# Kernel tuning notes

Hardware: AMD Instinct MI355X
Metric: run time of the kernel (lower is better)

## Reference

```python
import jax, jax.numpy as jnp
import numpy as np

N_NODES = 100000
N_EDGES = 1600000
IN_DIM, HID_DIM, OUT_DIM = 128, 128, 64


def setup_inputs() -> dict:
    key = jax.random.key(0)
    k1, k2, k3, k4 = jax.random.split(key, 4)
    x = jax.random.normal(k1, (N_NODES, IN_DIM), dtype=jnp.float32)
    edge_index = jax.random.randint(k2, (2, N_EDGES), 0, N_NODES, dtype=jnp.int32)
    # Glorot-ish init for weights
    W1 = jax.random.normal(k3, (IN_DIM, HID_DIM), dtype=jnp.float32) / np.sqrt(IN_DIM)
    W2 = jax.random.normal(k4, (HID_DIM, OUT_DIM), dtype=jnp.float32) / np.sqrt(HID_DIM)
    b1 = jnp.zeros((HID_DIM,), dtype=jnp.float32)
    b2 = jnp.zeros((OUT_DIM,), dtype=jnp.float32)
    return {"x": x, "edge_index": edge_index, "W1": W1, "b1": b1, "W2": W2, "b2": b2}


def _gcn_norm(edge_index, num_nodes):
    # PyG gcn_norm: add self-loops, symmetric normalization deg^-1/2 A deg^-1/2
    loops = jnp.arange(num_nodes, dtype=edge_index.dtype)
    src = jnp.concatenate([edge_index[0], loops])  # [E+N]
    tgt = jnp.concatenate([edge_index[1], loops])
    deg = jax.ops.segment_sum(jnp.ones_like(tgt, dtype=jnp.float32), tgt,
                              num_segments=num_nodes)
    dinv = jnp.where(deg > 0, jax.lax.rsqrt(deg), 0.0)
    norm = dinv[src] * dinv[tgt]  # [E+N]
    return src, tgt, norm


def _gcn_conv(x, W, b, src, tgt, norm, num_nodes):
    h = x @ W                              # [N, D_out] transform first (GCNConv order)
    msg = norm[:, None] * h[src]           # gather + scale per edge
    agg = jax.ops.segment_sum(msg, tgt, num_segments=num_nodes)  # scatter-add
    return agg + b


def reference(x, edge_index, W1, b1, W2, b2):
    n = x.shape[0]
    src, tgt, norm = _gcn_norm(edge_index, n)
    h = jax.nn.relu(_gcn_conv(x, W1, b1, src, tgt, norm, n))
    out = _gcn_conv(h, W2, b2, src, tgt, norm, n)
    return out
```

## Files before the change

### kernel.cpp

```cpp
#include <hip/hip_runtime.h>


typedef unsigned int uint;
typedef unsigned short ushort;
typedef __attribute__((ext_vector_type(8))) short bf16x8;
typedef __attribute__((ext_vector_type(4))) float f32x4;

#define BSHIFT 8
#define MAXBK  512
#define NB     256

__device__ inline ushort f2bf(float f) {
    uint u = __float_as_uint(f);
    return (ushort)((u + 0x7fffu + ((u >> 16) & 1u)) >> 16);
}
__device__ inline float bf_lo(uint u) { return __uint_as_float(u << 16); }
__device__ inline float bf_hi(uint u) { return __uint_as_float(u & 0xffff0000u); }

__global__ __launch_bounds__(256) void hist_kernel(const int* __restrict__ tgt,
                                                   int* __restrict__ counts,
                                                   int E, int chunk, int nbk) {
    __shared__ int hist[MAXBK];
    int t = threadIdx.x, b = blockIdx.x;
    for (int i = t; i < nbk; i += 256) hist[i] = 0;
    __syncthreads();
    int s = b * chunk, e = min(E, s + chunk);
    for (int i = s + t; i < e; i += 256) atomicAdd(&hist[tgt[i] >> BSHIFT], 1);
    __syncthreads();
    for (int i = t; i < nbk; i += 256) counts[i * NB + b] = hist[i];
}

__global__ __launch_bounds__(256) void scan_partial(const int* __restrict__ in,
                                                    int* __restrict__ bsum, int M) {
    int t = threadIdx.x, b = blockIdx.x;
    int base = b * 1024 + t * 4;
    int s = 0;
#pragma unroll
    for (int k = 0; k < 4; ++k) s += (base + k < M) ? in[base + k] : 0;
#pragma unroll
    for (int off = 32; off > 0; off >>= 1) s += __shfl_down(s, off, 64);
    __shared__ int ws[4];
    if ((t & 63) == 0) ws[t >> 6] = s;
    __syncthreads();
    if (t == 0) bsum[b] = ws[0] + ws[1] + ws[2] + ws[3];
}

__global__ __launch_bounds__(256) void scan_final_counts(int* __restrict__ counts,
                                                         const int* __restrict__ bsum,
                                                         int M) {
    int t = threadIdx.x, b = blockIdx.x;
    int lane = t & 63, wid = t >> 6;
    int p = 0;
    for (int i = t; i < b; i += 256) p += bsum[i];
#pragma unroll
    for (int off = 32; off > 0; off >>= 1) p += __shfl_down(p, off, 64);
    __shared__ int ps[4];
    if (lane == 0) ps[wid] = p;
    __syncthreads();
    int pre = ps[0] + ps[1] + ps[2] + ps[3];

    int base = b * 1024 + t * 4;
    int d[4];
#pragma unroll
    for (int k = 0; k < 4; ++k) d[k] = (base + k < M) ? counts[base + k] : 0;
    int tot = d[0] + d[1] + d[2] + d[3];
    int incl = tot;
#pragma unroll
    for (int off = 1; off < 64; off <<= 1) {
        int u = __shfl_up(incl, off, 64);
        if (lane >= off) incl += u;
    }
    __shared__ int wsum[4];
    if (lane == 63) wsum[wid] = incl;
    __syncthreads();
    int woff = 0;
    for (int w = 0; w < wid; ++w) woff += wsum[w];
    int run = incl - tot + woff + pre;
#pragma unroll
    for (int k = 0; k < 4; ++k) {
        if (base + k < M) counts[base + k] = run;
        run += d[k];
    }
}

__global__ __launch_bounds__(256) void bucket_scatter(const int* __restrict__ src,
                                                      const int* __restrict__ tgt,
                                                      const int* __restrict__ offsets,
                                                      int* __restrict__ tmpP,
                                                      int E, int chunk, int nbk) {
    __shared__ int cur[MAXBK];
    int t = threadIdx.x, b = blockIdx.x;
    for (int i = t; i < nbk; i += 256) cur[i] = offsets[i * NB + b];
    __syncthreads();
    int s = b * chunk, e = min(E, s + chunk);
    for (int i = s + t; i < e; i += 256) {
        int tg = tgt[i];
        int p = atomicAdd(&cur[tg >> BSHIFT], 1);
        tmpP[p] = (src[i] << BSHIFT) | (tg & 255);
    }
}

__global__ __launch_bounds__(256) void bucket_deg(const int* __restrict__ tmpP,
                                                  const int* __restrict__ offsets,
                                                  int* __restrict__ deg,
                                                  int N, int E, int nbk) {
    __shared__ int cnt[256];
    int t = threadIdx.x, b = blockIdx.x;
    cnt[t] = 0;
    __syncthreads();
    int s = offsets[b * NB];
    int e = (b + 1 < nbk) ? offsets[(b + 1) * NB] : E;
    for (int i = s + t; i < e; i += 256) atomicAdd(&cnt[tmpP[i] & 255], 1);
    __syncthreads();
    int node = b * 256 + t;
    if (node < N) deg[node] = cnt[t];
}

__global__ __launch_bounds__(256) void scan_final_deg(const int* __restrict__ deg,
                                                      const int* __restrict__ offsets,
                                                      int* __restrict__ rowptr,
                                                      float* __restrict__ dinv,
                                                      int N, int E) {
    int t = threadIdx.x, b = blockIdx.x;
    int lane = t & 63, wid = t >> 6;
    int pre = offsets[(4 * b) * NB];
    int base = b * 1024 + t * 4;
    int d[4];
#pragma unroll
    for (int k = 0; k < 4; ++k) d[k] = (base + k < N) ? deg[base + k] : 0;
    int tot = d[0] + d[1] + d[2] + d[3];
    int incl = tot;
#pragma unroll
    for (int off = 1; off < 64; off <<= 1) {
        int u = __shfl_up(incl, off, 64);
        if (lane >= off) incl += u;
    }
    __shared__ int wsum[4];
    if (lane == 63) wsum[wid] = incl;
    __syncthreads();
    int woff = 0;
    for (int w = 0; w < wid; ++w) woff += wsum[w];
    int run = incl - tot + woff + pre;
#pragma unroll
    for (int k = 0; k < 4; ++k) {
        if (base + k < N) {
            rowptr[base + k] = run;
            dinv[base + k] = rsqrtf((float)d[k] + 1.0f);
        }
        run += d[k];
    }
    if (b == gridDim.x - 1 && t == 255) rowptr[N] = E;
}

__global__ __launch_bounds__(256) void bucket_fill(const int* __restrict__ tmpP,
                                                   const int* __restrict__ rowptr,
                                                   int* __restrict__ csr_src, int N) {
    __shared__ int cur[256];
    int t = threadIdx.x, b = blockIdx.x;
    int base = b * 256;
    int node = base + t;
    if (node < N) cur[t] = rowptr[node];
    __syncthreads();
    int s = rowptr[base];
    int e = rowptr[min(base + 256, N)];
    for (int i = s + t; i < e; i += 256) {
        int ed = tmpP[i];
        int p = atomicAdd(&cur[ed & 255], 1);
        csr_src[p] = ed >> BSHIFT;
    }
}

template <int M>
__global__ __launch_bounds__(256) void gemm_mfma(const float* __restrict__ A,
                                                 const float* __restrict__ W,
                                                 ushort* __restrict__ C, int N) {
    constexpr int WTS = 136;
    __shared__ ushort WT[M * WTS];
    const int tid = threadIdx.x;
    for (int i = tid; i < 128 * (M / 4); i += 256) {
        int k = i / (M / 4);
        int n0 = (i % (M / 4)) * 4;
        float4 w = *(const float4*)&W[k * M + n0];
        WT[(n0 + 0) * WTS + k] = f2bf(w.x);
        WT[(n0 + 1) * WTS + k] = f2bf(w.y);
        WT[(n0 + 2) * WTS + k] = f2bf(w.z);
        WT[(n0 + 3) * WTS + k] = f2bf(w.w);
    }
    __syncthreads();

    const int wv = tid >> 6, lane = tid & 63;
    const int quad = lane >> 4, mrow = lane & 15;
    int arow_i = blockIdx.x * 64 + wv * 16 + mrow;
    if (arow_i >= N) arow_i = N - 1;
    const float* arow = &A[(size_t)arow_i * 128];

    f32x4 acc[M / 16];
#pragma unroll
    for (int t = 0; t < M / 16; ++t) acc[t] = (f32x4){0.f, 0.f, 0.f, 0.f};

#pragma unroll
    for (int ks = 0; ks < 4; ++ks) {
        const int k0 = ks * 32 + quad * 8;
        float4 a0 = *(const float4*)&arow[k0];
        float4 a1 = *(const float4*)&arow[k0 + 4];
        bf16x8 af;
        af[0] = (short)f2bf(a0.x); af[1] = (short)f2bf(a0.y);
        af[2] = (short)f2bf(a0.z); af[3] = (short)f2bf(a0.w);
        af[4] = (short)f2bf(a1.x); af[5] = (short)f2bf(a1.y);
        af[6] = (short)f2bf(a1.z); af[7] = (short)f2bf(a1.w);
#pragma unroll
        for (int t = 0; t < M / 16; ++t) {
            int n = t * 16 + mrow;
            bf16x8 bfr = *(const bf16x8*)&WT[n * WTS + k0];
            acc[t] = __builtin_amdgcn_mfma_f32_16x16x32_bf16(af, bfr, acc[t], 0, 0, 0);
        }
    }

    const int orow0 = blockIdx.x * 64 + wv * 16 + quad * 4;
#pragma unroll
    for (int r = 0; r < 4; ++r) {
        int orow = orow0 + r;
        if (orow < N) {
#pragma unroll
            for (int t = 0; t < M / 16; ++t)
                C[(size_t)orow * M + t * 16 + mrow] = f2bf(acc[t][r]);
        }
    }
}

template <int D, bool RELU>
__global__ __launch_bounds__(256) void gather_kernel(
    const ushort* __restrict__ h, const int* __restrict__ rowptr,
    const int* __restrict__ csr_src, const float* __restrict__ dinv,
    const float* __restrict__ bias, float* __restrict__ out, int N) {
    constexpr int Q = D / 8;
    constexpr int G = 64 / Q;
    const int wid = threadIdx.x >> 6, lane = threadIdx.x & 63;
    const int node = blockIdx.x * 4 + wid;
    if (node >= N) return;
    const int g = lane / Q, q = lane % Q;
    const int qoff = q * 8;
    const int beg = rowptr[node], end = rowptr[node + 1];
    float acc[8] = {};

    for (int j = beg; j < end; j += 2 * G) {
        int e0 = j + g, e1 = j + G + g;
        {
            bool v = e0 < end;
            int s = v ? csr_src[e0] : node;
            float w = v ? dinv[s] : 0.0f;
            uint4 hv = *(const uint4*)&h[(size_t)s * D + qoff];
            acc[0] += w * bf_lo(hv.x); acc[1] += w * bf_hi(hv.x);
            acc[2] += w * bf_lo(hv.y); acc[3] += w * bf_hi(hv.y);
            acc[4] += w * bf_lo(hv.z); acc[5] += w * bf_hi(hv.z);
            acc[6] += w * bf_lo(hv.w); acc[7] += w * bf_hi(hv.w);
        }
        {
            bool v = e1 < end;
            int s = v ? csr_src[e1] : node;
            float w = v ? dinv[s] : 0.0f;
            uint4 hv = *(const uint4*)&h[(size_t)s * D + qoff];
            acc[0] += w * bf_lo(hv.x); acc[1] += w * bf_hi(hv.x);
            acc[2] += w * bf_lo(hv.y); acc[3] += w * bf_hi(hv.y);
            acc[4] += w * bf_lo(hv.z); acc[5] += w * bf_hi(hv.z);
            acc[6] += w * bf_lo(hv.w); acc[7] += w * bf_hi(hv.w);
        }
    }
#pragma unroll
    for (int m = Q; m < 64; m <<= 1)
#pragma unroll
        for (int k = 0; k < 8; ++k) acc[k] += __shfl_xor(acc[k], m, 64);

    const float di = dinv[node];
    {
        uint4 hv = *(const uint4*)&h[(size_t)node * D + qoff];
        acc[0] += di * bf_lo(hv.x); acc[1] += di * bf_hi(hv.x);
        acc[2] += di * bf_lo(hv.y); acc[3] += di * bf_hi(hv.y);
        acc[4] += di * bf_lo(hv.z); acc[5] += di * bf_hi(hv.z);
        acc[6] += di * bf_lo(hv.w); acc[7] += di * bf_hi(hv.w);
    }
    if (g == 0) {
        float4 b0 = *(const float4*)&bias[qoff];
        float4 b1 = *(const float4*)&bias[qoff + 4];
        float r[8] = {di * acc[0] + b0.x, di * acc[1] + b0.y,
                      di * acc[2] + b0.z, di * acc[3] + b0.w,
                      di * acc[4] + b1.x, di * acc[5] + b1.y,
                      di * acc[6] + b1.z, di * acc[7] + b1.w};
        if (RELU) {
#pragma unroll
            for (int k = 0; k < 8; ++k) r[k] = fmaxf(r[k], 0.0f);
        }
        *(float4*)&out[(size_t)node * D + qoff]     = make_float4(r[0], r[1], r[2], r[3]);
        *(float4*)&out[(size_t)node * D + qoff + 4] = make_float4(r[4], r[5], r[6], r[7]);
    }
}

extern "C" void kernel_launch(void* const* d_in, const int* in_sizes, int n_in,
                              void* d_out, int out_size, void* d_ws, size_t ws_size,
                              hipStream_t stream) {
    const float* x  = (const float*)d_in[0];
    const int*   ei = (const int*)d_in[1];
    const float* W1 = (const float*)d_in[2];
    const float* b1 = (const float*)d_in[3];
    const float* W2 = (const float*)d_in[4];
    const float* b2 = (const float*)d_in[5];
    float* out = (float*)d_out;

    const int N = in_sizes[0] / 128;
    const int E = in_sizes[1] / 2;
    const int* src = ei;
    const int* tgt = ei + E;

    const int nbk   = (N + 255) >> BSHIFT;
    const int chunk = (E + NB - 1) / NB;
    const int Mc    = nbk * NB;

    float* ws = (float*)d_ws;
    const size_t Np = (size_t)((N + 3) & ~3);
    float*  dinv    = ws;
    int*    deg     = (int*)(ws + Np);
    int*    rowptr  = deg + Np;
    int*    counts  = rowptr + Np + 4;
    int*    bsum    = counts + MAXBK * NB;
    int*    csr_src = bsum + 128;
    int*    tmpP    = csr_src + E;
    ushort* h       = (ushort*)(tmpP + E);
    float*  h1      = (float*)(h + (size_t)N * 128);
    ushort* h2      = h;

    const int nbc = (Mc + 1023) / 1024;
    const int nbd = (N + 1023) / 1024;

    hist_kernel<<<NB, 256, 0, stream>>>(tgt, counts, E, chunk, nbk);
    scan_partial<<<nbc, 256, 0, stream>>>(counts, bsum, Mc);
    scan_final_counts<<<nbc, 256, 0, stream>>>(counts, bsum, Mc);
    bucket_scatter<<<NB, 256, 0, stream>>>(src, tgt, counts, tmpP, E, chunk, nbk);
    bucket_deg<<<nbk, 256, 0, stream>>>(tmpP, counts, deg, N, E, nbk);
    scan_final_deg<<<nbd, 256, 0, stream>>>(deg, counts, rowptr, dinv, N, E);
    bucket_fill<<<nbk, 256, 0, stream>>>(tmpP, rowptr, csr_src, N);

    gemm_mfma<128><<<(N + 63) / 64, 256, 0, stream>>>(x, W1, h, N);
    gather_kernel<128, true><<<(N + 3) / 4, 256, 0, stream>>>(
        h, rowptr, csr_src, dinv, b1, h1, N);

    gemm_mfma<64><<<(N + 63) / 64, 256, 0, stream>>>(h1, W2, h2, N);
    gather_kernel<64, false><<<(N + 3) / 4, 256, 0, stream>>>(
        h2, rowptr, csr_src, dinv, b2, out, N);
}
```

Measured before the change: 335.1 us.

## Fuse CSR build kernels and store hidden layer as bf16

Merges the per-bucket degree count, the degree scan and the CSR fill into one kernel that stages each bucket's packed edges in shared memory. This removes two launches and a second global read of the packed edges. The first-layer gather output is also written as bf16 instead of fp32 and read straight into the second GEMM, which roughly halves that intermediate's traffic and skips the conversion step. The large shared staging buffer lowers occupancy, and the extra bf16 rounding of the hidden activations adds some precision loss.

```diff
diff --git a/kernel.cpp b/kernel.cpp
--- a/kernel.cpp
+++ b/kernel.cpp
@@ -4,11 +4,13 @@
 typedef unsigned int uint;
 typedef unsigned short ushort;
 typedef __attribute__((ext_vector_type(8))) short bf16x8;
+typedef __attribute__((ext_vector_type(8))) ushort u16x8;
 typedef __attribute__((ext_vector_type(4))) float f32x4;
 
 #define BSHIFT 8
 #define MAXBK  512
 #define NB     256
+#define CAP    8192
 
 __device__ inline ushort f2bf(float f) {
     uint u = __float_as_uint(f);
@@ -100,78 +102,57 @@
     }
 }
 
-__global__ __launch_bounds__(256) void bucket_deg(const int* __restrict__ tmpP,
-                                                  const int* __restrict__ offsets,
-                                                  int* __restrict__ deg,
-                                                  int N, int E, int nbk) {
+__global__ __launch_bounds__(256) void bucket_finish(const int* __restrict__ tmpP,
+                                                     const int* __restrict__ offsets,
+                                                     int* __restrict__ rowptr,
+                                                     float* __restrict__ dinv,
+                                                     int* __restrict__ csr_src,
+                                                     int N, int E, int nbk) {
+    __shared__ int stage[CAP];
     __shared__ int cnt[256];
+    __shared__ int wsum[4];
     int t = threadIdx.x, b = blockIdx.x;
     cnt[t] = 0;
     __syncthreads();
     int s = offsets[b * NB];
     int e = (b + 1 < nbk) ? offsets[(b + 1) * NB] : E;
-    for (int i = s + t; i < e; i += 256) atomicAdd(&cnt[tmpP[i] & 255], 1);
-    __syncthreads();
-    int node = b * 256 + t;
-    if (node < N) deg[node] = cnt[t];
-}
-
-__global__ __launch_bounds__(256) void scan_final_deg(const int* __restrict__ deg,
-                                                      const int* __restrict__ offsets,
-                                                      int* __restrict__ rowptr,
-                                                      float* __restrict__ dinv,
-                                                      int N, int E) {
-    int t = threadIdx.x, b = blockIdx.x;
+    int m = e - s;
+    for (int i = t; i < m; i += 256) {
+        int ed = tmpP[s + i];
+        if (i < CAP) stage[i] = ed;
+        atomicAdd(&cnt[ed & 255], 1);
+    }
+    __syncthreads();
     int lane = t & 63, wid = t >> 6;
-    int pre = offsets[(4 * b) * NB];
-    int base = b * 1024 + t * 4;
-    int d[4];
-#pragma unroll
-    for (int k = 0; k < 4; ++k) d[k] = (base + k < N) ? deg[base + k] : 0;
-    int tot = d[0] + d[1] + d[2] + d[3];
-    int incl = tot;
+    int d = cnt[t];
+    int incl = d;
 #pragma unroll
     for (int off = 1; off < 64; off <<= 1) {
         int u = __shfl_up(incl, off, 64);
         if (lane >= off) incl += u;
     }
-    __shared__ int wsum[4];
     if (lane == 63) wsum[wid] = incl;
     __syncthreads();
     int woff = 0;
     for (int w = 0; w < wid; ++w) woff += wsum[w];
-    int run = incl - tot + woff + pre;
-#pragma unroll
-    for (int k = 0; k < 4; ++k) {
-        if (base + k < N) {
-            rowptr[base + k] = run;
-            dinv[base + k] = rsqrtf((float)d[k] + 1.0f);
-        }
-        run += d[k];
-    }
-    if (b == gridDim.x - 1 && t == 255) rowptr[N] = E;
-}
-
-__global__ __launch_bounds__(256) void bucket_fill(const int* __restrict__ tmpP,
-                                                   const int* __restrict__ rowptr,
-                                                   int* __restrict__ csr_src, int N) {
-    __shared__ int cur[256];
-    int t = threadIdx.x, b = blockIdx.x;
-    int base = b * 256;
-    int node = base + t;
-    if (node < N) cur[t] = rowptr[node];
-    __syncthreads();
-    int s = rowptr[base];
-    int e = rowptr[min(base + 256, N)];
-    for (int i = s + t; i < e; i += 256) {
-        int ed = tmpP[i];
-        int p = atomicAdd(&cur[ed & 255], 1);
+    int excl = s + incl - d + woff;
+    int node = b * 256 + t;
+    if (node < N) {
+        rowptr[node] = excl;
+        dinv[node] = rsqrtf((float)d + 1.0f);
+    }
+    if (b == nbk - 1 && t == 255) rowptr[N] = E;
+    cnt[t] = excl;
+    __syncthreads();
+    for (int i = t; i < m; i += 256) {
+        int ed = (i < CAP) ? stage[i] : tmpP[s + i];
+        int p = atomicAdd(&cnt[ed & 255], 1);
         csr_src[p] = ed >> BSHIFT;
     }
 }
 
-template <int M>
-__global__ __launch_bounds__(256) void gemm_mfma(const float* __restrict__ A,
+template <int M, typename AT>
+__global__ __launch_bounds__(256) void gemm_mfma(const AT* __restrict__ A,
                                                  const float* __restrict__ W,
                                                  ushort* __restrict__ C, int N) {
     constexpr int WTS = 136;
@@ -192,7 +173,7 @@
     const int quad = lane >> 4, mrow = lane & 15;
     int arow_i = blockIdx.x * 64 + wv * 16 + mrow;
     if (arow_i >= N) arow_i = N - 1;
-    const float* arow = &A[(size_t)arow_i * 128];
+    const AT* arow = &A[(size_t)arow_i * 128];
 
     f32x4 acc[M / 16];
 #pragma unroll
@@ -201,13 +182,17 @@
 #pragma unroll
     for (int ks = 0; ks < 4; ++ks) {
         const int k0 = ks * 32 + quad * 8;
-        float4 a0 = *(const float4*)&arow[k0];
-        float4 a1 = *(const float4*)&arow[k0 + 4];
         bf16x8 af;
-        af[0] = (short)f2bf(a0.x); af[1] = (short)f2bf(a0.y);
-        af[2] = (short)f2bf(a0.z); af[3] = (short)f2bf(a0.w);
-        af[4] = (short)f2bf(a1.x); af[5] = (short)f2bf(a1.y);
-        af[6] = (short)f2bf(a1.z); af[7] = (short)f2bf(a1.w);
+        if constexpr (sizeof(AT) == 4) {
+            float4 a0 = *(const float4*)&arow[k0];
+            float4 a1 = *(const float4*)&arow[k0 + 4];
+            af[0] = (short)f2bf(a0.x); af[1] = (short)f2bf(a0.y);
+            af[2] = (short)f2bf(a0.z); af[3] = (short)f2bf(a0.w);
+            af[4] = (short)f2bf(a1.x); af[5] = (short)f2bf(a1.y);
+            af[6] = (short)f2bf(a1.z); af[7] = (short)f2bf(a1.w);
+        } else {
+            af = *(const bf16x8*)&arow[k0];
+        }
 #pragma unroll
         for (int t = 0; t < M / 16; ++t) {
             int n = t * 16 + mrow;
@@ -228,11 +213,11 @@
     }
 }
 
-template <int D, bool RELU>
+template <int D, bool RELU, bool OUTBF>
 __global__ __launch_bounds__(256) void gather_kernel(
     const ushort* __restrict__ h, const int* __restrict__ rowptr,
     const int* __restrict__ csr_src, const float* __restrict__ dinv,
-    const float* __restrict__ bias, float* __restrict__ out, int N) {
+    const float* __restrict__ bias, void* __restrict__ outv, int N) {
     constexpr int Q = D / 8;
     constexpr int G = 64 / Q;
     const int wid = threadIdx.x >> 6, lane = threadIdx.x & 63;
@@ -290,8 +275,17 @@
 #pragma unroll
             for (int k = 0; k < 8; ++k) r[k] = fmaxf(r[k], 0.0f);
         }
-        *(float4*)&out[(size_t)node * D + qoff]     = make_float4(r[0], r[1], r[2], r[3]);
-        *(float4*)&out[(size_t)node * D + qoff + 4] = make_float4(r[4], r[5], r[6], r[7]);
+        if constexpr (OUTBF) {
+            ushort* out = (ushort*)outv;
+            u16x8 o;
+#pragma unroll
+            for (int k = 0; k < 8; ++k) o[k] = f2bf(r[k]);
+            *(u16x8*)&out[(size_t)node * D + qoff] = o;
+        } else {
+            float* out = (float*)outv;
+            *(float4*)&out[(size_t)node * D + qoff]     = make_float4(r[0], r[1], r[2], r[3]);
+            *(float4*)&out[(size_t)node * D + qoff + 4] = make_float4(r[4], r[5], r[6], r[7]);
+        }
     }
 }
 
@@ -318,32 +312,28 @@
     float* ws = (float*)d_ws;
     const size_t Np = (size_t)((N + 3) & ~3);
     float*  dinv    = ws;
-    int*    deg     = (int*)(ws + Np);
-    int*    rowptr  = deg + Np;
+    int*    rowptr  = (int*)(ws + Np);
     int*    counts  = rowptr + Np + 4;
     int*    bsum    = counts + MAXBK * NB;
     int*    csr_src = bsum + 128;
     int*    tmpP    = csr_src + E;
     ushort* h       = (ushort*)(tmpP + E);
-    float*  h1      = (float*)(h + (size_t)N * 128);
+    ushort* h1      = h + (size_t)N * 128;
     ushort* h2      = h;
 
     const int nbc = (Mc + 1023) / 1024;
-    const int nbd = (N + 1023) / 1024;
 
     hist_kernel<<<NB, 256, 0, stream>>>(tgt, counts, E, chunk, nbk);
     scan_partial<<<nbc, 256, 0, stream>>>(counts, bsum, Mc);
     scan_final_counts<<<nbc, 256, 0, stream>>>(counts, bsum, Mc);
     bucket_scatter<<<NB, 256, 0, stream>>>(src, tgt, counts, tmpP, E, chunk, nbk);
-    bucket_deg<<<nbk, 256, 0, stream>>>(tmpP, counts, deg, N, E, nbk);
-    scan_final_deg<<<nbd, 256, 0, stream>>>(deg, counts, rowptr, dinv, N, E);
-    bucket_fill<<<nbk, 256, 0, stream>>>(tmpP, rowptr, csr_src, N);
-
-    gemm_mfma<128><<<(N + 63) / 64, 256, 0, stream>>>(x, W1, h, N);
-    gather_kernel<128, true><<<(N + 3) / 4, 256, 0, stream>>>(
+    bucket_finish<<<nbk, 256, 0, stream>>>(tmpP, counts, rowptr, dinv, csr_src, N, E, nbk);
+
+    gemm_mfma<128, float><<<(N + 63) / 64, 256, 0, stream>>>(x, W1, h, N);
+    gather_kernel<128, true, true><<<(N + 3) / 4, 256, 0, stream>>>(
         h, rowptr, csr_src, dinv, b1, h1, N);
 
-    gemm_mfma<64><<<(N + 63) / 64, 256, 0, stream>>>(h1, W2, h2, N);
-    gather_kernel<64, false><<<(N + 3) / 4, 256, 0, stream>>>(
+    gemm_mfma<64, ushort><<<(N + 63) / 64, 256, 0, stream>>>(h1, W2, h2, N);
+    gather_kernel<64, false, false><<<(N + 3) / 4, 256, 0, stream>>>(
         h2, rowptr, csr_src, dinv, b2, out, N);
 }
```

Result: faster. 324.0 us (-3.3%).
